# Kernel optimization log

Measured on AMD Instinct MI355X. Metric: run time of the kernel, lower is better.

## Reference

```python
import jax, jax.numpy as jnp
import numpy as np

DIM = 384
H = 6
D = DIM // H
MLP = 4 * DIM
SCALE = D ** -0.5
LN_EPS = 1e-5


def _ln(x, w, b):
    m = jnp.mean(x, axis=-1, keepdims=True)
    v = jnp.mean((x - m) ** 2, axis=-1, keepdims=True)
    return (x - m) * jax.lax.rsqrt(v + LN_EPS) * w + b


def setup_inputs() -> dict:
    key = jax.random.key(0)
    ks = jax.random.split(key, 8)
    B, N = 8, 1024
    x = jax.random.normal(ks[0], (B, N, DIM), dtype=jnp.float32)
    # torch nn.Linear weights are [out, in]
    qkv_w = jax.random.normal(ks[1], (3 * DIM, DIM), dtype=jnp.float32) * (DIM ** -0.5)
    proj_w = jax.random.normal(ks[2], (DIM, DIM), dtype=jnp.float32) * (DIM ** -0.5)
    proj_b = jnp.zeros((DIM,), jnp.float32)
    # L2Q params, 'quadratic' init
    alpha = jnp.full((H, 1, 1), 0.125, jnp.float32)
    beta = jnp.full((H, 1, 1), 0.5, jnp.float32)
    gamma = jnp.zeros((H, 1, 1), jnp.float32)
    ln1_w = jnp.ones((DIM,), jnp.float32)
    ln1_b = jnp.zeros((DIM,), jnp.float32)
    ln2_w = jnp.ones((DIM,), jnp.float32)
    ln2_b = jnp.zeros((DIM,), jnp.float32)
    w1 = jax.random.normal(ks[3], (MLP, DIM), dtype=jnp.float32) * (DIM ** -0.5)
    b1 = jnp.zeros((MLP,), jnp.float32)
    w2 = jax.random.normal(ks[4], (DIM, MLP), dtype=jnp.float32) * (MLP ** -0.5)
    b2 = jnp.zeros((DIM,), jnp.float32)
    return {"x": x, "qkv_w": qkv_w, "proj_w": proj_w, "proj_b": proj_b,
            "alpha": alpha, "beta": beta, "gamma": gamma,
            "ln1_w": ln1_w, "ln1_b": ln1_b, "ln2_w": ln2_w, "ln2_b": ln2_b,
            "w1": w1, "b1": b1, "w2": w2, "b2": b2}


def reference(x, qkv_w, proj_w, proj_b, alpha, beta, gamma,
              ln1_w, ln1_b, ln2_w, ln2_b, w1, b1, w2, b2):
    B, N, C = x.shape
    # --- L2Q attention on LN(x) ---
    h = _ln(x, ln1_w, ln1_b)
    qkv = (h @ qkv_w.T).reshape(B, N, 3, H, D)
    q = qkv[:, :, 0].transpose(0, 2, 1, 3)  # [B,H,N,D]
    k = qkv[:, :, 1].transpose(0, 2, 1, 3)
    v = qkv[:, :, 2].transpose(0, 2, 1, 3)
    logits = jnp.einsum('bhnd,bhmd->bhnm', q, k) * SCALE
    attn = jax.nn.relu(alpha * logits ** 2 + beta * logits + gamma)
    attn = attn / (jnp.sum(attn, axis=-1, keepdims=True) + 1e-6)
    out = jnp.einsum('bhnm,bhmd->bhnd', attn, v)
    out = out.transpose(0, 2, 1, 3).reshape(B, N, C)
    x = x + out @ proj_w.T + proj_b
    # --- MLP on LN(x), exact GELU (torch default) ---
    h2 = _ln(x, ln2_w, ln2_b)
    m = jax.nn.gelu(h2 @ w1.T + b1, approximate=False)
    x = x + m @ w2.T + b2
    return x
```

## Files before the change

### kernel.cpp

```cpp
#include <hip/hip_runtime.h>
#include <hip/hip_bf16.h>
#include <math.h>

#define DIMC 384
#define NH 6
#define HD 64
#define MLPD 1536
#define BS 8
#define SEQ 1024
#define T_TOK (BS*SEQ)
#define TC ((size_t)T_TOK*DIMC)
#define QK_SCALE 0.125f

typedef __bf16 bf16;
typedef bf16 bf16x4 __attribute__((ext_vector_type(4)));
typedef bf16 bf16x8 __attribute__((ext_vector_type(8)));
typedef float floatx4 __attribute__((ext_vector_type(4)));

__device__ __forceinline__ void async_cp16(const void* gsrc, void* ldst) {
    __builtin_amdgcn_global_load_lds(
        (const __attribute__((address_space(1))) unsigned int*)gsrc,
        (__attribute__((address_space(3))) unsigned int*)ldst,
        16, 0, 0);
}

__global__ __launch_bounds__(256)
void prep_kernel(const float* __restrict__ s0, const float* __restrict__ s1,
                 const float* __restrict__ s2, const float* __restrict__ s3,
                 bf16* __restrict__ dst,
                 const float* __restrict__ x, const float* __restrict__ lw,
                 const float* __restrict__ lb, bf16* __restrict__ out) {
    if (blockIdx.x < 1728) {
        int i = blockIdx.x * 256 + threadIdx.x;
        const int n0 = 110592, n1 = 36864, n2 = 147456;
        const float4* src; int j;
        if (i < n0)           { src = (const float4*)s0; j = i; }
        else if (i < n0+n1)   { src = (const float4*)s1; j = i - n0; }
        else if (i < n0+n1+n2){ src = (const float4*)s2; j = i - n0 - n1; }
        else                  { src = (const float4*)s3; j = i - n0 - n1 - n2; }
        float4 v = src[j];
        bf16x4 o; o[0] = (bf16)v.x; o[1] = (bf16)v.y; o[2] = (bf16)v.z; o[3] = (bf16)v.w;
        ((bf16x4*)dst)[i] = o;
    } else {
        int row = (blockIdx.x - 1728) * 4 + (threadIdx.x >> 6);
        int t = threadIdx.x & 63;
        const float* xr = x + (size_t)row * DIMC;
        float vals[6];
        float s = 0.f;
        #pragma unroll
        for (int i = 0; i < 6; i++) { vals[i] = xr[t + i*64]; s += vals[i]; }
        #pragma unroll
        for (int m = 32; m; m >>= 1) s += __shfl_xor(s, m);
        float mean = s * (1.0f / DIMC);
        float sq = 0.f;
        #pragma unroll
        for (int i = 0; i < 6; i++) { float d = vals[i] - mean; sq += d * d; }
        #pragma unroll
        for (int m = 32; m; m >>= 1) sq += __shfl_xor(sq, m);
        float rstd = rsqrtf(sq * (1.0f / DIMC) + 1e-5f);
        bf16* orow = out + (size_t)row * DIMC;
        #pragma unroll
        for (int i = 0; i < 6; i++) {
            int c = t + i*64;
            orow[c] = (bf16)((vals[i] - mean) * rstd * lw[c] + lb[c]);
        }
    }
}

__global__ __launch_bounds__(256)
void ln2_fused(const float* __restrict__ x, const bf16* __restrict__ p0,
               const bf16* __restrict__ p1, const float* __restrict__ pb,
               const float* __restrict__ w, const float* __restrict__ b,
               float* __restrict__ x1, bf16* __restrict__ h) {
    int row = blockIdx.x * 4 + (threadIdx.x >> 6);
    int t = threadIdx.x & 63;
    size_t base = (size_t)row * DIMC;
    float vals[6];
    float s = 0.f;
    #pragma unroll
    for (int i = 0; i < 6; i++) {
        int c = t + i*64;
        float v = x[base + c] + (float)p0[base + c] + (float)p1[base + c] + pb[c];
        vals[i] = v; s += v;
    }
    #pragma unroll
    for (int m = 32; m; m >>= 1) s += __shfl_xor(s, m);
    float mean = s * (1.0f / DIMC);
    float sq = 0.f;
    #pragma unroll
    for (int i = 0; i < 6; i++) { float d = vals[i] - mean; sq += d * d; }
    #pragma unroll
    for (int m = 32; m; m >>= 1) sq += __shfl_xor(sq, m);
    float rstd = rsqrtf(sq * (1.0f / DIMC) + 1e-5f);
    #pragma unroll
    for (int i = 0; i < 6; i++) {
        int c = t + i*64;
        x1[base + c] = vals[i];
        h[base + c] = (bf16)((vals[i] - mean) * rstd * w[c] + b[c]);
    }
}

__global__ __launch_bounds__(256)
void reduce4(float* __restrict__ xo, const bf16* __restrict__ p0, const bf16* __restrict__ p1,
             const bf16* __restrict__ p2, const bf16* __restrict__ p3,
             const float* __restrict__ b2) {
    int i = blockIdx.x * 256 + threadIdx.x;
    float4 v = ((const float4*)xo)[i];
    int c = (i % 96) * 4;
    float4 bb = *(const float4*)(b2 + c);
    bf16x4 a0 = ((const bf16x4*)p0)[i], a1 = ((const bf16x4*)p1)[i];
    bf16x4 a2 = ((const bf16x4*)p2)[i], a3 = ((const bf16x4*)p3)[i];
    v.x += bb.x + (float)a0[0] + (float)a1[0] + (float)a2[0] + (float)a3[0];
    v.y += bb.y + (float)a0[1] + (float)a1[1] + (float)a2[1] + (float)a3[1];
    v.z += bb.z + (float)a0[2] + (float)a1[2] + (float)a2[2] + (float)a3[2];
    v.w += bb.w + (float)a0[3] + (float)a1[3] + (float)a2[3] + (float)a3[3];
    ((float4*)xo)[i] = v;
}

enum { EPI_NONE = 0, EPI_QKV = 1, EPI_GELU = 3 };

template<int EPI, int K, int KS, int NX, typename OutT>
__global__ __launch_bounds__(512)
void gemm_bt(const bf16* __restrict__ A, const bf16* __restrict__ W,
             const float* __restrict__ bias, OutT* out, int M, int N) {
    __shared__ __align__(16) bf16 Ash[3][4096];
    __shared__ __align__(16) bf16 Bsh[3][4096];
    constexpr int KB = K / KS;
    constexpr int NK = KB / 32;
    int L = blockIdx.x;
    int xcd = L & 7, ii = L >> 3;
    int ysub = ii & 7, rest = ii >> 3;
    int bx = rest % NX, bz = rest / NX;
    int by = ysub * 8 + xcd;
    int tid = threadIdx.x;
    int lane = tid & 63, w = tid >> 6;
    int quad = lane >> 4, l16 = lane & 15;
    int wr = w >> 2, wc = w & 3;
    int rbase = by * 128 + wr * 64;
    int cbase = bx * 128 + wc * 32;
    int kbase = bz * KB;
    const bf16* Ag1 = A + (size_t)(by*128 + (tid >> 2)) * K + kbase + (tid & 3) * 8;
    const bf16* Wg1 = W + (size_t)(bx*128 + (tid >> 2)) * K + kbase + (tid & 3) * 8;

    int arow = wr * 64;
    int brow = wc * 32;

    #define GSTAGE(KK, B) { async_cp16(Ag1 + (KK)*32, &Ash[B][tid*8]); \
                            async_cp16(Wg1 + (KK)*32, &Bsh[B][tid*8]); }
    GSTAGE(0, 0);
    GSTAGE(1, 1);

    floatx4 acc[4][2] = {};
    #pragma unroll 3
    for (int kk = 0; kk < NK; kk++) {
        if (kk + 1 < NK)
            asm volatile("s_waitcnt vmcnt(2)\n\ts_barrier" ::: "memory");
        else
            asm volatile("s_waitcnt vmcnt(0)\n\ts_barrier" ::: "memory");
        if (kk + 2 < NK) GSTAGE(kk+2, (kk+2)%3);
        const bf16* Ab = Ash[kk%3];
        const bf16* Bb = Bsh[kk%3];
        bf16x8 a[4], bfr[2];
        #pragma unroll
        for (int tm = 0; tm < 4; tm++)
            a[tm] = *(const bf16x8*)&Ab[(arow + tm*16 + l16) * 32 + quad*8];
        #pragma unroll
        for (int tn = 0; tn < 2; tn++)
            bfr[tn] = *(const bf16x8*)&Bb[(brow + tn*16 + l16) * 32 + quad*8];
        #pragma unroll
        for (int tm = 0; tm < 4; tm++)
            #pragma unroll
            for (int tn = 0; tn < 2; tn++)
                acc[tm][tn] = __builtin_amdgcn_mfma_f32_16x16x32_bf16(a[tm], bfr[tn], acc[tm][tn], 0, 0, 0);
    }
    #undef GSTAGE

    #pragma unroll
    for (int tm = 0; tm < 4; tm++)
        #pragma unroll
        for (int tn = 0; tn < 2; tn++) {
            if constexpr (EPI == EPI_QKV) {
                int colb = cbase + tn*16 + l16;
                int which = colb / 384;
                int rowb = rbase + tm*16 + quad*4;
                int bb = rowb >> 10;
                if (which == 2) {
                    int rem = colb - 768;
                    int hh = rem >> 6, d = rem & 63;
                    int n = rowb & 1023;
                    bf16x4 pk;
                    #pragma unroll
                    for (int r = 0; r < 4; r++) pk[r] = (bf16)acc[tm][tn][r];
                    *(bf16x4*)((bf16*)out + 2*TC + (((size_t)(bb*NH + hh) * HD + d) << 10) + n) = pk;
                } else {
                    int rem = colb - which*384;
                    int hh = rem >> 6, d = rem & 63;
                    #pragma unroll
                    for (int r = 0; r < 4; r++) {
                        int n = (rowb & 1023) + r;
                        ((bf16*)out)[(size_t)which*TC + (((size_t)(bb*NH + hh) * SEQ + n) << 6) + d]
                            = (bf16)acc[tm][tn][r];
                    }
                }
            } else if constexpr (EPI == EPI_NONE) {
                OutT* ob = out + (size_t)bz * M * N;
                #pragma unroll
                for (int r = 0; r < 4; r++) {
                    int row = rbase + tm*16 + quad*4 + r;
                    int col = cbase + tn*16 + l16;
                    ob[(size_t)row * N + col] = (OutT)acc[tm][tn][r];
                }
            } else {
                #pragma unroll
                for (int r = 0; r < 4; r++) {
                    int row = rbase + tm*16 + quad*4 + r;
                    int col = cbase + tn*16 + l16;
                    float v = acc[tm][tn][r] + bias[col];
                    v = 0.5f * v * (1.0f + erff(v * 0.70710678118f));
                    out[(size_t)row * N + col] = (OutT)v;
                }
            }
        }
}

__global__ __launch_bounds__(256)
void attn_kernel(const bf16* __restrict__ q, const bf16* __restrict__ k,
                 const bf16* __restrict__ vt, const float* __restrict__ alpha,
                 const float* __restrict__ beta, const float* __restrict__ gamma,
                 bf16* __restrict__ attn_out) {
    __shared__ __align__(16) bf16 smem[3][8192];

    int L = blockIdx.x;
    int xcd = L & 7, slot = L >> 3;
    int qt = slot & 15;
    int bh = xcd + ((slot >> 4) << 3);
    int bb = bh / NH, h = bh % NH;
    int q0 = qt * 64;
    int tid = threadIdx.x;
    int w = tid >> 6, lane = tid & 63, quad = lane >> 4, l16 = lane & 15;
    float av = alpha[h] * (QK_SCALE * QK_SCALE), bv = beta[h] * QK_SCALE, gv = gamma[h];
    const bf16* qb  = q  + (size_t)bh * SEQ * HD;
    const bf16* kb  = k  + (size_t)bh * SEQ * HD;
    const bf16* vtb = vt + (size_t)bh * HD * SEQ;

    bf16x8 qa[2];
    #pragma unroll
    for (int s = 0; s < 2; s++)
        qa[s] = *(const bf16x8*)(qb + (size_t)(q0 + w*16 + l16) * HD + s*32 + quad*8);

    floatx4 o[4] = {};
    float rsp = 0.f;
    int krow0 = ((l16 >> 2) << 3) + (l16 & 3);

    #define STAGE(CK, BUF)                                                              \
        {                                                                               \
            bf16* Kb_ = smem[BUF];                                                      \
            bf16* Vb_ = smem[BUF] + 4096;                                               \
            _Pragma("unroll")                                                           \
            for (int call = 0; call < 2; call++) {                                      \
                int i2 = call*256 + tid;                                                \
                int r_ = i2 >> 3, c_ = i2 & 7;                                          \
                int kk_ = (r_ & 3) | (((r_ >> 4) & 1) << 2);                            \
                async_cp16(kb  + (size_t)((CK) + r_) * HD + ((c_ ^ kk_) << 3),          \
                           Kb_ + i2*8);                                                 \
                async_cp16(vtb + (size_t)r_ * SEQ + (CK) + ((c_ ^ (r_ & 7)) << 3),      \
                           Vb_ + i2*8);                                                 \
            }                                                                           \
        }

    STAGE(0, 0);
    STAGE(64, 1);

    for (int c = 0; c < 16; c++) {
        if (c + 1 < 16)
            asm volatile("s_waitcnt vmcnt(4)\n\ts_barrier" ::: "memory");
        else
            asm volatile("s_waitcnt vmcnt(0)\n\ts_barrier" ::: "memory");
        if (c + 2 < 16) STAGE((c+2)*64, (c+2)%3);
        const bf16* Kb = smem[c%3];
        const bf16* Vb = smem[c%3] + 4096;
        floatx4 sb[2][2] = {};
        #pragma unroll
        for (int s = 0; s < 2; s++)
            #pragma unroll
            for (int b = 0; b < 2; b++)
                #pragma unroll
                for (int j = 0; j < 2; j++) {
                    int g = b*32 + j*4 + krow0;
                    int kk = (g & 3) | (((g >> 4) & 1) << 2);
                    bf16x8 kf = *(const bf16x8*)(Kb + g*64 + (((s*4 + quad) ^ kk) << 3));
                    sb[b][j] = __builtin_amdgcn_mfma_f32_16x16x32_bf16(kf, qa[s], sb[b][j], 0, 0, 0);
                }
        bf16x8 pf[2];
        #pragma unroll
        for (int b = 0; b < 2; b++)
            #pragma unroll
            for (int j = 0; j < 2; j++)
                #pragma unroll
                for (int r = 0; r < 4; r++) {
                    float xx = sb[b][j][r];
                    float p = fmaxf((av*xx + bv)*xx + gv, 0.f);
                    rsp += p;
                    pf[b][j*4 + r] = (bf16)p;
                }
        #pragma unroll
        for (int b = 0; b < 2; b++)
            #pragma unroll
            for (int d = 0; d < 4; d++) {
                int dr = d*16 + l16;
                bf16x8 vf = *(const bf16x8*)(Vb + dr*64 + ((((b<<2) + quad) ^ (dr & 7)) << 3));
                o[d] = __builtin_amdgcn_mfma_f32_16x16x32_bf16(pf[b], vf, o[d], 0, 0, 0);
            }
    }

    rsp += __shfl_xor(rsp, 16);
    rsp += __shfl_xor(rsp, 32);
    float rsd[4];
    #pragma unroll
    for (int r = 0; r < 4; r++)
        rsd[r] = __shfl(rsp, quad*4 + r) + 1e-6f;
    #pragma unroll
    for (int d = 0; d < 4; d++)
        #pragma unroll
        for (int r = 0; r < 4; r++) {
            int n = q0 + w*16 + quad*4 + r;
            attn_out[((size_t)(bb*SEQ + n)) * DIMC + h*HD + d*16 + l16] =
                (bf16)(o[d][r] / rsd[r]);
        }
    #undef STAGE
}

extern "C" void kernel_launch(void* const* d_in, const int* in_sizes, int n_in,
                              void* d_out, int out_size, void* d_ws, size_t ws_size,
                              hipStream_t stream) {
    const float* x      = (const float*)d_in[0];
    const float* qkv_w  = (const float*)d_in[1];
    const float* proj_w = (const float*)d_in[2];
    const float* proj_b = (const float*)d_in[3];
    const float* alpha  = (const float*)d_in[4];
    const float* beta   = (const float*)d_in[5];
    const float* gamma  = (const float*)d_in[6];
    const float* ln1_w  = (const float*)d_in[7];
    const float* ln1_b  = (const float*)d_in[8];
    const float* ln2_w  = (const float*)d_in[9];
    const float* ln2_b  = (const float*)d_in[10];
    const float* w1     = (const float*)d_in[11];
    const float* b1     = (const float*)d_in[12];
    const float* w2     = (const float*)d_in[13];
    const float* b2     = (const float*)d_in[14];
    float* out = (float*)d_out;

    char* base = (char*)d_ws;
    bf16* wq_bf = (bf16*)base;
    bf16* wp_bf = wq_bf + 442368;
    bf16* w1_bf = wq_bf + 589824;
    bf16* w2_bf = wq_bf + 1179648;
    bf16* h      = (bf16*)(base + 3538944);
    bf16* qkv    = (bf16*)(base + 9830400);
    bf16* attn_o = (bf16*)(base + 28704768);
    bf16* m      = qkv;
    bf16* Pp     = (bf16*)(base + 34996224);
    bf16* Pm     = (bf16*)(base + 34996224);

    prep_kernel<<<1728 + T_TOK/4, 256, 0, stream>>>(
        qkv_w, proj_w, w1, w2, wq_bf, x, ln1_w, ln1_b, h);
    gemm_bt<EPI_QKV, 384, 1, 9, bf16><<<64*9, 512, 0, stream>>>(
        h, wq_bf, nullptr, qkv, T_TOK, 1152);
    attn_kernel<<<768, 256, 0, stream>>>(
        qkv, qkv + TC, qkv + 2*TC, alpha, beta, gamma, attn_o);
    gemm_bt<EPI_NONE, 384, 2, 3, bf16><<<64*3*2, 512, 0, stream>>>(
        attn_o, wp_bf, nullptr, Pp, T_TOK, DIMC);
    ln2_fused<<<T_TOK/4, 256, 0, stream>>>(x, Pp, Pp + TC, proj_b, ln2_w, ln2_b, out, h);
    gemm_bt<EPI_GELU, 384, 1, 12, bf16><<<64*12, 512, 0, stream>>>(
        h, w1_bf, b1, m, T_TOK, MLPD);
    gemm_bt<EPI_NONE, 1536, 4, 3, bf16><<<64*3*4, 512, 0, stream>>>(
        m, w2_bf, nullptr, Pm, T_TOK, DIMC);
    reduce4<<<TC/4/256, 256, 0, stream>>>(out, Pm, Pm + TC, Pm + 2*TC, Pm + 3*TC, b2);
}
```

Baseline: 197.3 us.

## Fuse split-K reduction into final GEMM via atomic tile counters, drop reduce4

Removes the separate reduce4 kernel. The last split-K block for each output tile, found through an atomic counter that prep_kernel zeroes, sums the partial bf16 results, adds the bias and the residual, and writes the fp32 output. The split-K factor for the W2 GEMM also drops from 4 to 3, leaving fewer partials and fewer blocks. This saves one kernel launch and one full pass over the partial buffers, but it relies on threadfence ordering, and the tail reduction runs serially in whichever block finishes last.

```diff
diff --git a/kernel.cpp b/kernel.cpp
--- a/kernel.cpp
+++ b/kernel.cpp
@@ -29,7 +29,8 @@
                  const float* __restrict__ s2, const float* __restrict__ s3,
                  bf16* __restrict__ dst,
                  const float* __restrict__ x, const float* __restrict__ lw,
-                 const float* __restrict__ lb, bf16* __restrict__ out) {
+                 const float* __restrict__ lb, bf16* __restrict__ out,
+                 int* __restrict__ cnt) {
     if (blockIdx.x < 1728) {
         int i = blockIdx.x * 256 + threadIdx.x;
         const int n0 = 110592, n1 = 36864, n2 = 147456;
@@ -41,7 +42,7 @@
         float4 v = src[j];
         bf16x4 o; o[0] = (bf16)v.x; o[1] = (bf16)v.y; o[2] = (bf16)v.z; o[3] = (bf16)v.w;
         ((bf16x4*)dst)[i] = o;
-    } else {
+    } else if (blockIdx.x < 3776) {
         int row = (blockIdx.x - 1728) * 4 + (threadIdx.x >> 6);
         int t = threadIdx.x & 63;
         const float* xr = x + (size_t)row * DIMC;
@@ -64,6 +65,8 @@
             int c = t + i*64;
             orow[c] = (bf16)((vals[i] - mean) * rstd * lw[c] + lb[c]);
         }
+    } else {
+        if (threadIdx.x < 192) cnt[threadIdx.x] = 0;
     }
 }
 
@@ -100,29 +103,13 @@
     }
 }
 
-__global__ __launch_bounds__(256)
-void reduce4(float* __restrict__ xo, const bf16* __restrict__ p0, const bf16* __restrict__ p1,
-             const bf16* __restrict__ p2, const bf16* __restrict__ p3,
-             const float* __restrict__ b2) {
-    int i = blockIdx.x * 256 + threadIdx.x;
-    float4 v = ((const float4*)xo)[i];
-    int c = (i % 96) * 4;
-    float4 bb = *(const float4*)(b2 + c);
-    bf16x4 a0 = ((const bf16x4*)p0)[i], a1 = ((const bf16x4*)p1)[i];
-    bf16x4 a2 = ((const bf16x4*)p2)[i], a3 = ((const bf16x4*)p3)[i];
-    v.x += bb.x + (float)a0[0] + (float)a1[0] + (float)a2[0] + (float)a3[0];
-    v.y += bb.y + (float)a0[1] + (float)a1[1] + (float)a2[1] + (float)a3[1];
-    v.z += bb.z + (float)a0[2] + (float)a1[2] + (float)a2[2] + (float)a3[2];
-    v.w += bb.w + (float)a0[3] + (float)a1[3] + (float)a2[3] + (float)a3[3];
-    ((float4*)xo)[i] = v;
-}
-
-enum { EPI_NONE = 0, EPI_QKV = 1, EPI_GELU = 3 };
+enum { EPI_NONE = 0, EPI_QKV = 1, EPI_GELU = 3, EPI_RED = 5 };
 
 template<int EPI, int K, int KS, int NX, typename OutT>
 __global__ __launch_bounds__(512)
 void gemm_bt(const bf16* __restrict__ A, const bf16* __restrict__ W,
-             const float* __restrict__ bias, OutT* out, int M, int N) {
+             const float* __restrict__ bias, OutT* out, int M, int N,
+             float* fout, int* cnt) {
     __shared__ __align__(16) bf16 Ash[3][4096];
     __shared__ __align__(16) bf16 Bsh[3][4096];
     constexpr int KB = K / KS;
@@ -202,7 +189,7 @@
                             = (bf16)acc[tm][tn][r];
                     }
                 }
-            } else if constexpr (EPI == EPI_NONE) {
+            } else if constexpr (EPI == EPI_NONE || EPI == EPI_RED) {
                 OutT* ob = out + (size_t)bz * M * N;
                 #pragma unroll
                 for (int r = 0; r < 4; r++) {
@@ -221,6 +208,39 @@
                 }
             }
         }
+
+    if constexpr (EPI == EPI_RED) {
+        __syncthreads();
+        int* shl = (int*)Ash;
+        if (tid == 0) {
+            __threadfence();
+            shl[0] = atomicAdd(cnt + (by*NX + bx), 1);
+        }
+        __syncthreads();
+        if (shl[0] == KS - 1) {
+            __threadfence();
+            int rb = by * 128, cb = bx * 128;
+            #pragma unroll
+            for (int e = 0; e < 8; e++) {
+                int idx = e*2048 + tid*4;
+                int row = rb + (idx >> 7);
+                int col = cb + (idx & 127);
+                size_t off = (size_t)row * N + col;
+                float4 xv = *(float4*)(fout + off);
+                float4 bb4 = *(const float4*)(bias + col);
+                float s0 = xv.x + bb4.x, s1 = xv.y + bb4.y;
+                float s2 = xv.z + bb4.z, s3 = xv.w + bb4.w;
+                #pragma unroll
+                for (int z = 0; z < KS; z++) {
+                    bf16x4 pv = *(const bf16x4*)((const bf16*)out + (size_t)z*M*N + off);
+                    s0 += (float)pv[0]; s1 += (float)pv[1];
+                    s2 += (float)pv[2]; s3 += (float)pv[3];
+                }
+                float4 r; r.x = s0; r.y = s1; r.z = s2; r.w = s3;
+                *(float4*)(fout + off) = r;
+            }
+        }
+    }
 }
 
 __global__ __launch_bounds__(256)
@@ -361,19 +381,19 @@
     bf16* m      = qkv;
     bf16* Pp     = (bf16*)(base + 34996224);
     bf16* Pm     = (bf16*)(base + 34996224);
-
-    prep_kernel<<<1728 + T_TOK/4, 256, 0, stream>>>(
-        qkv_w, proj_w, w1, w2, wq_bf, x, ln1_w, ln1_b, h);
+    int*  cnt    = (int*)(base + 34996224 + 3*TC*2);
+
+    prep_kernel<<<3777, 256, 0, stream>>>(
+        qkv_w, proj_w, w1, w2, wq_bf, x, ln1_w, ln1_b, h, cnt);
     gemm_bt<EPI_QKV, 384, 1, 9, bf16><<<64*9, 512, 0, stream>>>(
-        h, wq_bf, nullptr, qkv, T_TOK, 1152);
+        h, wq_bf, nullptr, qkv, T_TOK, 1152, nullptr, nullptr);
     attn_kernel<<<768, 256, 0, stream>>>(
         qkv, qkv + TC, qkv + 2*TC, alpha, beta, gamma, attn_o);
     gemm_bt<EPI_NONE, 384, 2, 3, bf16><<<64*3*2, 512, 0, stream>>>(
-        attn_o, wp_bf, nullptr, Pp, T_TOK, DIMC);
+        attn_o, wp_bf, nullptr, Pp, T_TOK, DIMC, nullptr, nullptr);
     ln2_fused<<<T_TOK/4, 256, 0, stream>>>(x, Pp, Pp + TC, proj_b, ln2_w, ln2_b, out, h);
     gemm_bt<EPI_GELU, 384, 1, 12, bf16><<<64*12, 512, 0, stream>>>(
-        h, w1_bf, b1, m, T_TOK, MLPD);
-    gemm_bt<EPI_NONE, 1536, 4, 3, bf16><<<64*3*4, 512, 0, stream>>>(
-        m, w2_bf, nullptr, Pm, T_TOK, DIMC);
-    reduce4<<<TC/4/256, 256, 0, stream>>>(out, Pm, Pm + TC, Pm + 2*TC, Pm + 3*TC, b2);
-}
+        h, w1_bf, b1, m, T_TOK, MLPD, nullptr, nullptr);
+    gemm_bt<EPI_RED, 1536, 3, 3, bf16><<<64*3*3, 512, 0, stream>>>(
+        m, w2_bf, b2, Pm, T_TOK, DIMC, out, cnt);
+}
```

Measured after the change: 275.3 us. 1.4x slower.
